# Performance work log

Measured on AMD Instinct MI355X. Metric: run time of the kernel, lower is better.

The kernel has to match this reference:

```python
import jax, jax.numpy as jnp
import numpy as np

NGROUPS = 368
NMODELS = 16
BATCH = 16384

def setup_inputs() -> dict:
    key = jax.random.key(0)
    kx, kw, kb = jax.random.split(key, 3)
    x = jax.random.normal(kx, (BATCH, NGROUPS, NMODELS), dtype=jnp.float32)
    # 368 independent Linear(nmodels, 1): weight [368, nmodels], bias [368]
    bound = 1.0 / np.sqrt(NMODELS)
    W = jax.random.uniform(kw, (NGROUPS, NMODELS), minval=-bound, maxval=bound, dtype=jnp.float32)
    b = jax.random.uniform(kb, (NGROUPS,), minval=-bound, maxval=bound, dtype=jnp.float32)
    return {"x": x, "W": W, "b": b}

def reference(x, W, b):
    # Fused grouped dot: out[bg] = sum_n x[b,g,n] * W[g,n] + b[g]
    return jnp.einsum("bgn,gn->bg", x, W) + b
```

## Files before the change

### kernel.cpp

```cpp
#include <hip/hip_runtime.h>


#define NGROUPS 368
#define NMODELS 16

__global__ __launch_bounds__(256) void ensemble_kernel(
    const float* __restrict__ x,
    const float* __restrict__ W,
    const float* __restrict__ bias,
    float* __restrict__ out,
    int batch)
{
    const int rows = batch >> 2;
    const int total = rows * NGROUPS;
    const int stride = gridDim.x * blockDim.x;

    for (int idx = blockIdx.x * blockDim.x + threadIdx.x; idx < total; idx += stride) {
        const int g  = idx % NGROUPS;
        const int b0 = idx / NGROUPS;

        const float4* wp = reinterpret_cast<const float4*>(W + (size_t)g * NMODELS);
        const float4 w0 = wp[0], w1 = wp[1], w2 = wp[2], w3 = wp[3];
        const float bg = bias[g];

        #pragma unroll
        for (int j = 0; j < 4; ++j) {
            const int bb = b0 + j * rows;
            const size_t base = ((size_t)bb * NGROUPS + g) * NMODELS;
            const float4* xp = reinterpret_cast<const float4*>(x + base);
            const float4 x0 = xp[0], x1 = xp[1], x2 = xp[2], x3 = xp[3];

            float s = x0.x * w0.x + x0.y * w0.y + x0.z * w0.z + x0.w * w0.w;
            s += x1.x * w1.x + x1.y * w1.y + x1.z * w1.z + x1.w * w1.w;
            s += x2.x * w2.x + x2.y * w2.y + x2.z * w2.z + x2.w * w2.w;
            s += x3.x * w3.x + x3.y * w3.y + x3.z * w3.z + x3.w * w3.w;

            out[(size_t)bb * NGROUPS + g] = s + bg;
        }
    }
}

extern "C" void kernel_launch(void* const* d_in, const int* in_sizes, int n_in,
                              void* d_out, int out_size, void* d_ws, size_t ws_size,
                              hipStream_t stream)
{
    const float* x    = (const float*)d_in[0];
    const float* W    = (const float*)d_in[1];
    const float* bias = (const float*)d_in[2];
    float* out = (float*)d_out;

    const int batch = in_sizes[0] / (NGROUPS * NMODELS);

    const int rows  = batch >> 2;
    const int total = rows * NGROUPS;
    int blocks = (total + 255) / 256;
    if (blocks > 2048) blocks = 2048;

    ensemble_kernel<<<blocks, 256, 0, stream>>>(x, W, bias, out, batch);
}
```

Measured before the change: 89.83 us.

## Map one float4 per thread and reduce dot products with quad shuffles

Reassigns work so each thread loads a single contiguous float4 of x, giving fully coalesced wavefront loads instead of 64-byte strided per-thread reads. The four partial sums of each 16-wide dot product are combined with xor shuffles, and one lane per quad writes the output with bias. This adds shuffle and index arithmetic per element and leaves three quarters of lanes idle at the store.

```diff
diff --git a/kernel.cpp b/kernel.cpp
--- a/kernel.cpp
+++ b/kernel.cpp
@@ -2,40 +2,31 @@
 
 
 #define NGROUPS 368
-#define NMODELS 16
 
 __global__ __launch_bounds__(256) void ensemble_kernel(
-    const float* __restrict__ x,
-    const float* __restrict__ W,
+    const float4* __restrict__ x4,
+    const float4* __restrict__ w4,
     const float* __restrict__ bias,
     float* __restrict__ out,
-    int batch)
+    int totf4)
 {
-    const int rows = batch >> 2;
-    const int total = rows * NGROUPS;
-    const int stride = gridDim.x * blockDim.x;
+    const int tid    = blockIdx.x * 256 + threadIdx.x;
+    const int stride = gridDim.x * 256;
+    const int q      = tid & 3;
 
-    for (int idx = blockIdx.x * blockDim.x + threadIdx.x; idx < total; idx += stride) {
-        const int g  = idx % NGROUPS;
-        const int b0 = idx / NGROUPS;
+    #pragma unroll 4
+    for (int f = tid; f < totf4; f += stride) {
+        const float4 xv = x4[f];
+        const int o = f >> 2;
+        const int g = o % NGROUPS;
+        const float4 wv = w4[(g << 2) | q];
 
-        const float4* wp = reinterpret_cast<const float4*>(W + (size_t)g * NMODELS);
-        const float4 w0 = wp[0], w1 = wp[1], w2 = wp[2], w3 = wp[3];
-        const float bg = bias[g];
+        float s = xv.x * wv.x + xv.y * wv.y + xv.z * wv.z + xv.w * wv.w;
+        s += __shfl_xor(s, 1);
+        s += __shfl_xor(s, 2);
 
-        #pragma unroll
-        for (int j = 0; j < 4; ++j) {
-            const int bb = b0 + j * rows;
-            const size_t base = ((size_t)bb * NGROUPS + g) * NMODELS;
-            const float4* xp = reinterpret_cast<const float4*>(x + base);
-            const float4 x0 = xp[0], x1 = xp[1], x2 = xp[2], x3 = xp[3];
-
-            float s = x0.x * w0.x + x0.y * w0.y + x0.z * w0.z + x0.w * w0.w;
-            s += x1.x * w1.x + x1.y * w1.y + x1.z * w1.z + x1.w * w1.w;
-            s += x2.x * w2.x + x2.y * w2.y + x2.z * w2.z + x2.w * w2.w;
-            s += x3.x * w3.x + x3.y * w3.y + x3.z * w3.z + x3.w * w3.w;
-
-            out[(size_t)bb * NGROUPS + g] = s + bg;
+        if (q == 0) {
+            out[o] = s + bias[g];
         }
     }
 }
@@ -44,17 +35,15 @@
                               void* d_out, int out_size, void* d_ws, size_t ws_size,
                               hipStream_t stream)
 {
-    const float* x    = (const float*)d_in[0];
-    const float* W    = (const float*)d_in[1];
-    const float* bias = (const float*)d_in[2];
+    const float4* x4   = (const float4*)d_in[0];
+    const float4* w4   = (const float4*)d_in[1];
+    const float* bias  = (const float*)d_in[2];
     float* out = (float*)d_out;
 
-    const int batch = in_sizes[0] / (NGROUPS * NMODELS);
+    const int totf4 = in_sizes[0] >> 2;
 
-    const int rows  = batch >> 2;
-    const int total = rows * NGROUPS;
-    int blocks = (total + 255) / 256;
+    int blocks = (totf4 + 255) / 256;
     if (blocks > 2048) blocks = 2048;
 
-    ensemble_kernel<<<blocks, 256, 0, stream>>>(x, W, bias, out, batch);
+    ensemble_kernel<<<blocks, 256, 0, stream>>>(x4, w4, bias, out, totf4);
 }
```

After: 89.02 us. No clear change (-0.9%).
